# Kernel optimization log

Hardware: AMD Instinct MI355X
Metric: run time of the kernel (lower is better)

Reference implementation:

```python
import jax, jax.numpy as jnp
import numpy as np

N_NODES = 100000
N_EDGES = 1600000
IN_CH, HID, OUT_CH = 512, 16, 64


def setup_inputs() -> dict:
    key = jax.random.key(0)
    ks = jax.random.split(key, 9)
    x = jax.random.normal(ks[0], (N_NODES, IN_CH), dtype=jnp.float32)
    edge_index1 = jax.random.randint(ks[1], (2, N_EDGES), 0, N_NODES, dtype=jnp.int32)
    edge_weight1 = jax.random.uniform(ks[2], (N_EDGES,), dtype=jnp.float32)
    edge_index2 = jax.random.randint(ks[3], (2, N_EDGES), 0, N_NODES, dtype=jnp.int32)
    edge_weight2 = jax.random.uniform(ks[4], (N_EDGES,), dtype=jnp.float32)
    W1 = jax.random.normal(ks[5], (IN_CH, HID), dtype=jnp.float32) / np.sqrt(IN_CH)
    b1 = jnp.zeros((HID,), dtype=jnp.float32)
    W2 = jax.random.normal(ks[6], (HID, OUT_CH), dtype=jnp.float32) / np.sqrt(HID)
    b2 = jnp.zeros((OUT_CH,), dtype=jnp.float32)
    return dict(x=x, edge_index1=edge_index1, edge_weight1=edge_weight1,
                edge_index2=edge_index2, edge_weight2=edge_weight2,
                W1=W1, b1=b1, W2=W2, b2=b2, num_nodes=N_NODES)


def _gcn_conv(x, W, b, row, col, w, num_nodes):
    # symmetric-normalized GCN aggregation: out = D^-1/2 A D^-1/2 (x W) + b
    deg = jax.ops.segment_sum(w, row, num_segments=num_nodes)  # [N]
    dinv = jnp.where(deg > 0, jax.lax.rsqrt(jnp.maximum(deg, 1e-12)), 0.0)
    norm = dinv[row] * w * dinv[col]                            # [E]
    h = x @ W                                                   # [N, F_out]
    msg = norm[:, None] * h[col]                                # [E, F_out]
    return jax.ops.segment_sum(msg, row, num_segments=num_nodes) + b


def reference(x, edge_index1, edge_weight1, edge_index2, edge_weight2,
              W1, b1, W2, b2, num_nodes):
    # concat edge lists; torch_sparse.coalesce(op='add') merges duplicates by
    # summing weights — the subsequent degree + scatter-add aggregation is
    # invariant to that dedup, so we run directly on the concatenated list.
    ei = jnp.concatenate([edge_index1, edge_index2], axis=1)    # [2, 2E]
    ew = jnp.concatenate([edge_weight1, edge_weight2])          # [2E]
    row, col = ei[0], ei[1]
    h = _gcn_conv(x, W1, b1, row, col, ew, num_nodes)
    h = jax.nn.relu(h)  # dropout is identity in eval mode
    h = _gcn_conv(h, W2, b2, row, col, ew, num_nodes)
    return jax.nn.log_softmax(h, axis=1)
```

## Files before the change

kernel.cpp:

```cpp
#include <hip/hip_runtime.h>
#include <hip/hip_bf16.h>
#include <hip/hip_fp16.h>

#define IN_CH 512
#define HID 16
#define OUT_CH 64
#define CAP 20480
#define PE 8192

typedef __attribute__((ext_vector_type(8))) short bf16x8;
typedef __attribute__((ext_vector_type(4))) float f32x4;

__device__ inline unsigned short f2bf(float f) {
    unsigned int u = __float_as_uint(f);
    return (unsigned short)((u + 0x7fffu + ((u >> 16) & 1u)) >> 16);
}

union A8 { bf16x8 v; short2 p[4]; };
__device__ inline short2 pk2(float a, float b) {
    union { __hip_bfloat162 h; short2 s; } u;
    u.h = __float22bfloat162_rn(make_float2(a, b));
    return u.s;
}

__global__ void k_init(int* __restrict__ cursors, int nbk) {
    int i = threadIdx.x;
    if (i < nbk) cursors[i] = i * CAP;
}

__global__ __launch_bounds__(1024) void k_partition(const int* __restrict__ ei1, const float* __restrict__ w1, int E1,
                                                    const int* __restrict__ ei2, const float* __restrict__ w2, int E2,
                                                    int* __restrict__ cursors,
                                                    uint2* __restrict__ packed, int Et) {
    __shared__ int hist[256];
    __shared__ int sc[256];
    __shared__ int lbase[256];
    __shared__ int gbase[256];
    __shared__ int lcur[256];
    __shared__ uint2 stage[PE];
    __shared__ unsigned char bkt[PE];
    int tid = threadIdx.x;
    int e0 = blockIdx.x * PE;
    if (tid < 256) hist[tid] = 0;
    __syncthreads();
    int r[8];
    #pragma unroll
    for (int j = 0; j < 8; ++j) {
        int e = e0 + j * 1024 + tid;
        int rr = -1;
        if (e < Et) rr = (e < E1) ? ei1[e] : ei2[e - E1];
        r[j] = rr;
        if (rr >= 0) atomicAdd(&hist[rr >> 9], 1);
    }
    __syncthreads();
    int v = (tid < 256) ? hist[tid] : 0;
    if (tid < 256) sc[tid] = v;
    __syncthreads();
    for (int off = 1; off < 256; off <<= 1) {
        int t = (tid >= off && tid < 256) ? sc[tid - off] : 0;
        __syncthreads();
        if (tid < 256) sc[tid] += t;
        __syncthreads();
    }
    if (tid < 256) {
        int ex = sc[tid] - v;
        lbase[tid] = ex;
        lcur[tid] = ex;
        gbase[tid] = (v > 0) ? atomicAdd(&cursors[tid], v) : 0;
    }
    __syncthreads();
    #pragma unroll
    for (int j = 0; j < 8; ++j) {
        if (r[j] >= 0) {
            int e = e0 + j * 1024 + tid;
            int cc; float ww;
            if (e < E1) { cc = ei1[e + E1]; ww = w1[e]; }
            else        { int f = e - E1; cc = ei2[f + E2]; ww = w2[f]; }
            int bk = r[j] >> 9;
            int pos = atomicAdd(&lcur[bk], 1);
            stage[pos] = make_uint2(((unsigned)(r[j] & 511) << 17) | (unsigned)cc,
                                    __float_as_uint(ww));
            bkt[pos] = (unsigned char)bk;
        }
    }
    __syncthreads();
    int nv = min(PE, Et - e0);
    for (int i = tid; i < nv; i += 1024) {
        int bk = bkt[i];
        packed[(size_t)gbase[bk] + (i - lbase[bk])] = stage[i];
    }
}

__global__ void k_bucket_scan(const int* __restrict__ cursors, int* __restrict__ cbase, int nbk) {
    __shared__ int s[256];
    int tid = threadIdx.x;
    int v = (tid < nbk) ? (cursors[tid] - tid * CAP) : 0;
    s[tid] = v;
    __syncthreads();
    for (int off = 1; off < 256; off <<= 1) {
        int t = (tid >= off) ? s[tid - off] : 0;
        __syncthreads();
        s[tid] += t;
        __syncthreads();
    }
    if (tid < nbk) cbase[tid] = s[tid] - v;
}

__global__ __launch_bounds__(1024) void k_buildcsr(const uint2* __restrict__ packed,
                                                   const int* __restrict__ cursors,
                                                   const int* __restrict__ cbase,
                                                   int2* __restrict__ rowmeta,
                                                   float* __restrict__ dinv, int2* __restrict__ csr, int N) {
    __shared__ int lcnt[512];
    __shared__ int lcur[512];
    __shared__ int lscan[512];
    __shared__ float ldeg[512];
    int b = blockIdx.x, tid = threadIdx.x;
    int M = cursors[b] - b * CAP;
    const uint2* pk = packed + (size_t)b * CAP;
    if (tid < 512) { lcnt[tid] = 0; ldeg[tid] = 0.f; }
    __syncthreads();
    for (int i = tid; i < M; i += 1024) atomicAdd(&lcnt[pk[i].x >> 17], 1);
    __syncthreads();
    int v = (tid < 512) ? lcnt[tid] : 0;
    if (tid < 512) lscan[tid] = v;
    __syncthreads();
    for (int off = 1; off < 512; off <<= 1) {
        int t = (tid >= off && tid < 512) ? lscan[tid - off] : 0;
        __syncthreads();
        if (tid < 512) lscan[tid] += t;
        __syncthreads();
    }
    int cb = cbase[b];
    if (tid < 512) {
        int ex = lscan[tid] - v;
        lcur[tid] = cb + ex;
        int node = b * 512 + tid;
        if (node < N) rowmeta[node] = make_int2(cb + ex, v);
    }
    __syncthreads();
    for (int i = tid; i < M; i += 1024) {
        uint2 u = pk[i];
        int lr = u.x >> 17;
        int c  = u.x & 0x1FFFF;
        int p = atomicAdd(&lcur[lr], 1);
        csr[p] = make_int2(c, (int)u.y);
        atomicAdd(&ldeg[lr], __uint_as_float(u.y));
    }
    __syncthreads();
    if (tid < 512) {
        int node = b * 512 + tid;
        if (node < N) {
            float d = ldeg[tid];
            dinv[node] = (d > 0.f) ? rsqrtf(fmaxf(d, 1e-12f)) : 0.f;
        }
    }
}

__global__ void k_prep(const float* __restrict__ W1, unsigned short* __restrict__ W1s) {
    for (int p = threadIdx.x; p < 1024; p += 256) {
        int kc = p >> 6, lane = p & 63;
        int q = lane >> 4, m = lane & 15;
        int k0 = kc * 32 + q * 8;
        unsigned v[8];
        #pragma unroll
        for (int j = 0; j < 8; ++j) v[j] = f2bf(W1[(k0 + j) * HID + m]);
        uint4 o;
        o.x = v[0] | (v[1] << 16); o.y = v[2] | (v[3] << 16);
        o.z = v[4] | (v[5] << 16); o.w = v[6] | (v[7] << 16);
        ((uint4*)W1s)[p] = o;
    }
}

__global__ __launch_bounds__(256) void k_gemm1(const float* __restrict__ x,
                                               const unsigned short* __restrict__ W1s,
                                               const float* __restrict__ dinv,
                                               __half* __restrict__ h1s, int n) {
    int wave = threadIdx.x >> 6, lane = threadIdx.x & 63;
    int tiles = (n + 15) >> 4;
    int t = blockIdx.x * 4 + wave;
    if (t >= tiles) return;

    int m = lane & 15, quad = lane >> 4;

    const bf16x8* Wv = (const bf16x8*)W1s;
    bf16x8 Bf[16];
    #pragma unroll
    for (int kc = 0; kc < 16; ++kc) Bf[kc] = Wv[kc * 64 + lane];

    int row = t * 16 + m;
    int rl = min(row, n - 1);
    const float4* xr = (const float4*)(x + (size_t)rl * IN_CH + quad * 8);

    f32x4 acc = {0.f, 0.f, 0.f, 0.f};
    #pragma unroll
    for (int kc = 0; kc < 16; ++kc) {
        float4 v0 = xr[kc * 8];
        float4 v1 = xr[kc * 8 + 1];
        A8 a;
        a.p[0] = pk2(v0.x, v0.y); a.p[1] = pk2(v0.z, v0.w);
        a.p[2] = pk2(v1.x, v1.y); a.p[3] = pk2(v1.z, v1.w);
        acc = __builtin_amdgcn_mfma_f32_16x16x32_bf16(a.v, Bf[kc], acc, 0, 0, 0);
    }

    int base = t * 16 + quad * 4;
    #pragma unroll
    for (int r = 0; r < 4; ++r) {
        int orow = base + r;
        if (orow < n) h1s[(size_t)orow * HID + m] = __float2half(dinv[orow] * acc[r]);
    }
}

__global__ __launch_bounds__(256) void k_agg1(const __half* __restrict__ h1s,
                                              const int2* __restrict__ csr,
                                              const int2* __restrict__ rowmeta,
                                              const float* __restrict__ dinv,
                                              const float* __restrict__ b1,
                                              __half* __restrict__ out1s, int n) {
    int wave = threadIdx.x >> 6, lane = threadIdx.x & 63;
    int node = blockIdx.x * 4 + wave;
    if (node >= n) return;
    int slot = lane >> 2, c4 = lane & 3;
    int2 rm = rowmeta[node];
    const int2* ce = csr + rm.x;
    int deg = rm.y;
    f32x4 acc = {0.f, 0.f, 0.f, 0.f};
    for (int i = slot; i < deg; i += 16) {
        int2 e = ce[i];
        float w = __int_as_float(e.y);
        uint2 raw = ((const uint2*)(h1s + (size_t)e.x * HID))[c4];
        float2 f01 = __half22float2(*(const __half2*)&raw.x);
        float2 f23 = __half22float2(*(const __half2*)&raw.y);
        acc[0] = fmaf(w, f01.x, acc[0]); acc[1] = fmaf(w, f01.y, acc[1]);
        acc[2] = fmaf(w, f23.x, acc[2]); acc[3] = fmaf(w, f23.y, acc[3]);
    }
    #pragma unroll
    for (int off = 4; off < 64; off <<= 1) {
        acc[0] += __shfl_xor(acc[0], off, 64);
        acc[1] += __shfl_xor(acc[1], off, 64);
        acc[2] += __shfl_xor(acc[2], off, 64);
        acc[3] += __shfl_xor(acc[3], off, 64);
    }
    if (lane < 4) {
        float dv = dinv[node];
        float4 bb = ((const float4*)b1)[c4];
        float4 o;
        o.x = fmaxf(fmaf(dv, acc[0], bb.x), 0.f) * dv;
        o.y = fmaxf(fmaf(dv, acc[1], bb.y), 0.f) * dv;
        o.z = fmaxf(fmaf(dv, acc[2], bb.z), 0.f) * dv;
        o.w = fmaxf(fmaf(dv, acc[3], bb.w), 0.f) * dv;
        __half2 p01 = __float22half2_rn(make_float2(o.x, o.y));
        __half2 p23 = __float22half2_rn(make_float2(o.z, o.w));
        uint2 st;
        st.x = *(unsigned*)&p01; st.y = *(unsigned*)&p23;
        ((uint2*)(out1s + (size_t)node * HID))[c4] = st;
    }
}

__global__ __launch_bounds__(256) void k_layer2(const __half* __restrict__ out1s,
                                                const int2* __restrict__ csr,
                                                const int2* __restrict__ rowmeta,
                                                const float* __restrict__ dinv,
                                                const float* __restrict__ W2,
                                                const float* __restrict__ b2,
                                                float* __restrict__ out, int n) {
    __shared__ float W2l[HID * OUT_CH];
    for (int i = threadIdx.x; i < HID * OUT_CH; i += 256) W2l[i] = W2[i];
    __syncthreads();

    int wave = threadIdx.x >> 6, lane = threadIdx.x & 63;
    int node = blockIdx.x * 4 + wave;
    if (node >= n) return;
    int slot = lane >> 2, c4 = lane & 3;
    int2 rm = rowmeta[node];
    const int2* ce = csr + rm.x;
    int deg = rm.y;
    f32x4 acc = {0.f, 0.f, 0.f, 0.f};
    for (int i = slot; i < deg; i += 16) {
        int2 e = ce[i];
        float w = __int_as_float(e.y);
        uint2 raw = ((const uint2*)(out1s + (size_t)e.x * HID))[c4];
        float2 f01 = __half22float2(*(const __half2*)&raw.x);
        float2 f23 = __half22float2(*(const __half2*)&raw.y);
        acc[0] = fmaf(w, f01.x, acc[0]); acc[1] = fmaf(w, f01.y, acc[1]);
        acc[2] = fmaf(w, f23.x, acc[2]); acc[3] = fmaf(w, f23.y, acc[3]);
    }
    #pragma unroll
    for (int off = 4; off < 64; off <<= 1) {
        acc[0] += __shfl_xor(acc[0], off, 64);
        acc[1] += __shfl_xor(acc[1], off, 64);
        acc[2] += __shfl_xor(acc[2], off, 64);
        acc[3] += __shfl_xor(acc[3], off, 64);
    }
    float dv = dinv[node];
    acc[0] *= dv; acc[1] *= dv; acc[2] *= dv; acc[3] *= dv;
    float v = b2[lane];
    #pragma unroll
    for (int gg = 0; gg < 4; ++gg) {
        float a0 = __shfl(acc[0], gg, 64);
        float a1 = __shfl(acc[1], gg, 64);
        float a2 = __shfl(acc[2], gg, 64);
        float a3 = __shfl(acc[3], gg, 64);
        v = fmaf(a0, W2l[(4 * gg + 0) * OUT_CH + lane], v);
        v = fmaf(a1, W2l[(4 * gg + 1) * OUT_CH + lane], v);
        v = fmaf(a2, W2l[(4 * gg + 2) * OUT_CH + lane], v);
        v = fmaf(a3, W2l[(4 * gg + 3) * OUT_CH + lane], v);
    }
    float m = v;
    #pragma unroll
    for (int off = 32; off; off >>= 1) m = fmaxf(m, __shfl_xor(m, off, 64));
    float ex = __expf(v - m);
    float s = ex;
    #pragma unroll
    for (int off = 32; off; off >>= 1) s += __shfl_xor(s, off, 64);
    out[(size_t)node * OUT_CH + lane] = (v - m) - __logf(s);
}

extern "C" void kernel_launch(void* const* d_in, const int* in_sizes, int n_in,
                              void* d_out, int out_size, void* d_ws, size_t ws_size,
                              hipStream_t stream) {
    const float* x   = (const float*)d_in[0];
    const int*   ei1 = (const int*)d_in[1];
    const float* w1  = (const float*)d_in[2];
    const int*   ei2 = (const int*)d_in[3];
    const float* w2  = (const float*)d_in[4];
    const float* W1  = (const float*)d_in[5];
    const float* b1  = (const float*)d_in[6];
    const float* W2  = (const float*)d_in[7];
    const float* b2  = (const float*)d_in[8];
    int N  = in_sizes[0] / IN_CH;
    int E1 = in_sizes[2];
    int E2 = in_sizes[4];
    int Et = E1 + E2;
    float* out = (float*)d_out;
    int nbk = (N + 511) >> 9;

    char* p = (char*)d_ws;
    int*   cursors  = (int*)p;   p += 1024;
    int*   cbase    = (int*)p;   p += 1024;
    int2*  rowmeta  = (int2*)p;  p += (size_t)N * 8;
    float* dinv     = (float*)p; p += (size_t)N * 4;
    unsigned short* W1s = (unsigned short*)p; p += IN_CH * HID * 2;
    int2*  csr      = (int2*)p;  p += (size_t)Et * 8;
    uint2* packed   = (uint2*)p;
    __half* h1s     = (__half*)p;
    __half* out1s   = h1s + (size_t)N * HID;

    k_init<<<1, 256, 0, stream>>>(cursors, nbk);
    k_prep<<<1, 256, 0, stream>>>(W1, W1s);
    k_partition<<<(Et + PE - 1) / PE, 1024, 0, stream>>>(ei1, w1, E1, ei2, w2, E2,
                                                         cursors, packed, Et);
    k_bucket_scan<<<1, 256, 0, stream>>>(cursors, cbase, nbk);
    k_buildcsr<<<nbk, 1024, 0, stream>>>(packed, cursors, cbase,
                                         rowmeta, dinv, csr, N);
    int tiles = (N + 15) / 16;
    k_gemm1<<<(tiles + 3) / 4, 256, 0, stream>>>(x, W1s, dinv, h1s, N);
    k_agg1<<<(N + 3) / 4, 256, 0, stream>>>(h1s, csr, rowmeta, dinv, b1, out1s, N);
    k_layer2<<<(N + 3) / 4, 256, 0, stream>>>(out1s, csr, rowmeta, dinv, W2, b2, out, N);
}
```

Measured before the change: 502.2 us.

## Build CSR with global atomic histogram and scatter instead of bucketed partition

Replaces the two-pass bucket partition and shared-memory CSR build with a plain counting sort: global atomic histogram of row counts and degree sums, a two-level scan for row offsets, and an atomic scatter of edges into the CSR. The aggregation kernels recover each row's start from the post-scatter cursor minus its degree. This drops the packed staging buffer and the shared-memory staging, but it adds more kernel launches and relies on global atomics at random addresses across 3.2M edges, which may be contended or uncoalesced. The order of edges within a row is now nondeterministic.

```diff
diff --git a/kernel.cpp b/kernel.cpp
--- a/kernel.cpp
+++ b/kernel.cpp
@@ -5,8 +5,6 @@
 #define IN_CH 512
 #define HID 16
 #define OUT_CH 64
-#define CAP 20480
-#define PE 8192
 
 typedef __attribute__((ext_vector_type(8))) short bf16x8;
 typedef __attribute__((ext_vector_type(4))) float f32x4;
@@ -23,78 +21,52 @@
     return u.s;
 }
 
-__global__ void k_init(int* __restrict__ cursors, int nbk) {
-    int i = threadIdx.x;
-    if (i < nbk) cursors[i] = i * CAP;
-}
-
-__global__ __launch_bounds__(1024) void k_partition(const int* __restrict__ ei1, const float* __restrict__ w1, int E1,
-                                                    const int* __restrict__ ei2, const float* __restrict__ w2, int E2,
-                                                    int* __restrict__ cursors,
-                                                    uint2* __restrict__ packed, int Et) {
-    __shared__ int hist[256];
-    __shared__ int sc[256];
-    __shared__ int lbase[256];
-    __shared__ int gbase[256];
-    __shared__ int lcur[256];
-    __shared__ uint2 stage[PE];
-    __shared__ unsigned char bkt[PE];
-    int tid = threadIdx.x;
-    int e0 = blockIdx.x * PE;
-    if (tid < 256) hist[tid] = 0;
+__global__ void k_zero(int* __restrict__ cnt, float* __restrict__ degf, int N) {
+    int i = blockIdx.x * 256 + threadIdx.x;
+    if (i < N) { cnt[i] = 0; degf[i] = 0.f; }
+}
+
+__global__ void k_hist(const int* __restrict__ ei1, const float* __restrict__ w1, int E1,
+                       const int* __restrict__ ei2, const float* __restrict__ w2, int E2,
+                       int* __restrict__ cnt, float* __restrict__ degf, int Et) {
+    int e = blockIdx.x * 256 + threadIdx.x;
+    if (e >= Et) return;
+    int r; float w;
+    if (e < E1) { r = ei1[e]; w = w1[e]; }
+    else        { int f = e - E1; r = ei2[f]; w = w2[f]; }
+    atomicAdd(&cnt[r], 1);
+    atomicAdd(&degf[r], w);
+}
+
+__global__ __launch_bounds__(512) void k_scan1(const int* __restrict__ cnt,
+                                               const float* __restrict__ degf,
+                                               int2* __restrict__ rowmeta,
+                                               int* __restrict__ btot,
+                                               float* __restrict__ dinv, int N) {
+    __shared__ int s[512];
+    int b = blockIdx.x, tid = threadIdx.x;
+    int node = b * 512 + tid;
+    int v = (node < N) ? cnt[node] : 0;
+    s[tid] = v;
     __syncthreads();
-    int r[8];
-    #pragma unroll
-    for (int j = 0; j < 8; ++j) {
-        int e = e0 + j * 1024 + tid;
-        int rr = -1;
-        if (e < Et) rr = (e < E1) ? ei1[e] : ei2[e - E1];
-        r[j] = rr;
-        if (rr >= 0) atomicAdd(&hist[rr >> 9], 1);
-    }
-    __syncthreads();
-    int v = (tid < 256) ? hist[tid] : 0;
-    if (tid < 256) sc[tid] = v;
-    __syncthreads();
-    for (int off = 1; off < 256; off <<= 1) {
-        int t = (tid >= off && tid < 256) ? sc[tid - off] : 0;
+    for (int off = 1; off < 512; off <<= 1) {
+        int t = (tid >= off) ? s[tid - off] : 0;
         __syncthreads();
-        if (tid < 256) sc[tid] += t;
+        s[tid] += t;
         __syncthreads();
     }
-    if (tid < 256) {
-        int ex = sc[tid] - v;
-        lbase[tid] = ex;
-        lcur[tid] = ex;
-        gbase[tid] = (v > 0) ? atomicAdd(&cursors[tid], v) : 0;
-    }
-    __syncthreads();
-    #pragma unroll
-    for (int j = 0; j < 8; ++j) {
-        if (r[j] >= 0) {
-            int e = e0 + j * 1024 + tid;
-            int cc; float ww;
-            if (e < E1) { cc = ei1[e + E1]; ww = w1[e]; }
-            else        { int f = e - E1; cc = ei2[f + E2]; ww = w2[f]; }
-            int bk = r[j] >> 9;
-            int pos = atomicAdd(&lcur[bk], 1);
-            stage[pos] = make_uint2(((unsigned)(r[j] & 511) << 17) | (unsigned)cc,
-                                    __float_as_uint(ww));
-            bkt[pos] = (unsigned char)bk;
-        }
-    }
-    __syncthreads();
-    int nv = min(PE, Et - e0);
-    for (int i = tid; i < nv; i += 1024) {
-        int bk = bkt[i];
-        packed[(size_t)gbase[bk] + (i - lbase[bk])] = stage[i];
-    }
-}
-
-__global__ void k_bucket_scan(const int* __restrict__ cursors, int* __restrict__ cbase, int nbk) {
+    if (node < N) {
+        rowmeta[node] = make_int2(s[tid] - v, v);
+        float d = degf[node];
+        dinv[node] = (d > 0.f) ? rsqrtf(fmaxf(d, 1e-12f)) : 0.f;
+    }
+    if (tid == 511) btot[b] = s[511];
+}
+
+__global__ void k_scan2(const int* __restrict__ btot, int* __restrict__ cbase, int nbk) {
     __shared__ int s[256];
     int tid = threadIdx.x;
-    int v = (tid < nbk) ? (cursors[tid] - tid * CAP) : 0;
+    int v = (tid < nbk) ? btot[tid] : 0;
     s[tid] = v;
     __syncthreads();
     for (int off = 1; off < 256; off <<= 1) {
@@ -106,55 +78,23 @@
     if (tid < nbk) cbase[tid] = s[tid] - v;
 }
 
-__global__ __launch_bounds__(1024) void k_buildcsr(const uint2* __restrict__ packed,
-                                                   const int* __restrict__ cursors,
-                                                   const int* __restrict__ cbase,
-                                                   int2* __restrict__ rowmeta,
-                                                   float* __restrict__ dinv, int2* __restrict__ csr, int N) {
-    __shared__ int lcnt[512];
-    __shared__ int lcur[512];
-    __shared__ int lscan[512];
-    __shared__ float ldeg[512];
-    int b = blockIdx.x, tid = threadIdx.x;
-    int M = cursors[b] - b * CAP;
-    const uint2* pk = packed + (size_t)b * CAP;
-    if (tid < 512) { lcnt[tid] = 0; ldeg[tid] = 0.f; }
-    __syncthreads();
-    for (int i = tid; i < M; i += 1024) atomicAdd(&lcnt[pk[i].x >> 17], 1);
-    __syncthreads();
-    int v = (tid < 512) ? lcnt[tid] : 0;
-    if (tid < 512) lscan[tid] = v;
-    __syncthreads();
-    for (int off = 1; off < 512; off <<= 1) {
-        int t = (tid >= off && tid < 512) ? lscan[tid - off] : 0;
-        __syncthreads();
-        if (tid < 512) lscan[tid] += t;
-        __syncthreads();
-    }
-    int cb = cbase[b];
-    if (tid < 512) {
-        int ex = lscan[tid] - v;
-        lcur[tid] = cb + ex;
-        int node = b * 512 + tid;
-        if (node < N) rowmeta[node] = make_int2(cb + ex, v);
-    }
-    __syncthreads();
-    for (int i = tid; i < M; i += 1024) {
-        uint2 u = pk[i];
-        int lr = u.x >> 17;
-        int c  = u.x & 0x1FFFF;
-        int p = atomicAdd(&lcur[lr], 1);
-        csr[p] = make_int2(c, (int)u.y);
-        atomicAdd(&ldeg[lr], __uint_as_float(u.y));
-    }
-    __syncthreads();
-    if (tid < 512) {
-        int node = b * 512 + tid;
-        if (node < N) {
-            float d = ldeg[tid];
-            dinv[node] = (d > 0.f) ? rsqrtf(fmaxf(d, 1e-12f)) : 0.f;
-        }
-    }
+__global__ void k_apply(int2* __restrict__ rowmeta, const int* __restrict__ cbase, int N) {
+    int node = blockIdx.x * 256 + threadIdx.x;
+    if (node >= N) return;
+    int2 rm = rowmeta[node];
+    rowmeta[node] = make_int2(rm.x + cbase[node >> 9], rm.y);
+}
+
+__global__ void k_scatter(const int* __restrict__ ei1, const float* __restrict__ w1, int E1,
+                          const int* __restrict__ ei2, const float* __restrict__ w2, int E2,
+                          int2* __restrict__ rowmeta, int2* __restrict__ csr, int Et) {
+    int e = blockIdx.x * 256 + threadIdx.x;
+    if (e >= Et) return;
+    int r, c; float w;
+    if (e < E1) { r = ei1[e]; c = ei1[e + E1]; w = w1[e]; }
+    else        { int f = e - E1; r = ei2[f]; c = ei2[f + E2]; w = w2[f]; }
+    int pos = atomicAdd(&((int*)rowmeta)[2 * r], 1);
+    csr[pos] = make_int2(c, (int)__float_as_uint(w));
 }
 
 __global__ void k_prep(const float* __restrict__ W1, unsigned short* __restrict__ W1s) {
@@ -222,8 +162,8 @@
     if (node >= n) return;
     int slot = lane >> 2, c4 = lane & 3;
     int2 rm = rowmeta[node];
-    const int2* ce = csr + rm.x;
     int deg = rm.y;
+    const int2* ce = csr + (rm.x - deg);
     f32x4 acc = {0.f, 0.f, 0.f, 0.f};
     for (int i = slot; i < deg; i += 16) {
         int2 e = ce[i];
@@ -273,8 +213,8 @@
     if (node >= n) return;
     int slot = lane >> 2, c4 = lane & 3;
     int2 rm = rowmeta[node];
-    const int2* ce = csr + rm.x;
     int deg = rm.y;
+    const int2* ce = csr + (rm.x - deg);
     f32x4 acc = {0.f, 0.f, 0.f, 0.f};
     for (int i = slot; i < deg; i += 16) {
         int2 e = ce[i];
@@ -336,23 +276,27 @@
     int nbk = (N + 511) >> 9;
 
     char* p = (char*)d_ws;
-    int*   cursors  = (int*)p;   p += 1024;
+    int*   cnt      = (int*)p;   p += (size_t)N * 4;
+    float* degf     = (float*)p; p += (size_t)N * 4;
+    int*   btot     = (int*)p;   p += 1024;
     int*   cbase    = (int*)p;   p += 1024;
     int2*  rowmeta  = (int2*)p;  p += (size_t)N * 8;
     float* dinv     = (float*)p; p += (size_t)N * 4;
     unsigned short* W1s = (unsigned short*)p; p += IN_CH * HID * 2;
     int2*  csr      = (int2*)p;  p += (size_t)Et * 8;
-    uint2* packed   = (uint2*)p;
-    __half* h1s     = (__half*)p;
-    __half* out1s   = h1s + (size_t)N * HID;
-
-    k_init<<<1, 256, 0, stream>>>(cursors, nbk);
+    __half* h1s     = (__half*)p; p += (size_t)N * HID * 2;
+    __half* out1s   = (__half*)p;
+
+    int egrid = (Et + 255) / 256;
+    int ngrid = (N + 255) / 256;
+
+    k_zero<<<ngrid, 256, 0, stream>>>(cnt, degf, N);
     k_prep<<<1, 256, 0, stream>>>(W1, W1s);
-    k_partition<<<(Et + PE - 1) / PE, 1024, 0, stream>>>(ei1, w1, E1, ei2, w2, E2,
-                                                         cursors, packed, Et);
-    k_bucket_scan<<<1, 256, 0, stream>>>(cursors, cbase, nbk);
-    k_buildcsr<<<nbk, 1024, 0, stream>>>(packed, cursors, cbase,
-                                         rowmeta, dinv, csr, N);
+    k_hist<<<egrid, 256, 0, stream>>>(ei1, w1, E1, ei2, w2, E2, cnt, degf, Et);
+    k_scan1<<<nbk, 512, 0, stream>>>(cnt, degf, rowmeta, btot, dinv, N);
+    k_scan2<<<1, 256, 0, stream>>>(btot, cbase, nbk);
+    k_apply<<<ngrid, 256, 0, stream>>>(rowmeta, cbase, N);
+    k_scatter<<<egrid, 256, 0, stream>>>(ei1, w1, E1, ei2, w2, E2, rowmeta, csr, Et);
     int tiles = (N + 15) / 16;
     k_gemm1<<<(tiles + 3) / 4, 256, 0, stream>>>(x, W1s, dinv, h1s, N);
     k_agg1<<<(N + 3) / 4, 256, 0, stream>>>(h1s, csr, rowmeta, dinv, b1, out1s, N);
```

Measured after the change: 970.3 us. 1.93x slower.
